# Kernel optimization log

Hardware: AMD Instinct MI355X
Metric: run time of the kernel (lower is better)

The kernel has to match this reference:

```python
import jax, jax.numpy as jnp
import numpy as np

B, C, S, DIM = 8, 3, 1024, 768
H = 3
HD = DIM // H  # 256


def setup_inputs() -> dict:
    key = jax.random.key(0)
    ks = jax.random.split(key, 7)
    s = 1.0 / np.sqrt(HD)  # torch Linear default init scale
    return {
        "linear_embed": jax.random.normal(ks[0], (B, C, S, DIM), dtype=jnp.float32),
        "Wq": jax.random.uniform(ks[1], (H, HD, HD), jnp.float32, -s, s),
        "bq": jax.random.uniform(ks[2], (H, HD), jnp.float32, -s, s),
        "Wk": jax.random.uniform(ks[3], (H, HD, HD), jnp.float32, -s, s),
        "bk": jax.random.uniform(ks[4], (H, HD), jnp.float32, -s, s),
        "Wv": jax.random.uniform(ks[5], (H, HD, HD), jnp.float32, -s, s),
        "bv": jax.random.uniform(ks[6], (H, HD), jnp.float32, -s, s),
    }


def reference(linear_embed, Wq, bq, Wk, bk, Wv, bv):
    # Split last dim into heads: [B, C, S, H, HD]
    x = linear_embed.reshape(B, C, S, H, HD)
    # Per-head Linear: y = x @ W.T + b (torch convention, W is [out, in])
    q = jnp.einsum("bcshd,hed->bcshe", x, Wq) + bq
    k = jnp.einsum("bcshd,hed->bcshe", x, Wk) + bk
    v = jnp.einsum("bcshd,hed->bcshe", x, Wv) + bv
    scale = 1.0 / np.sqrt(HD)
    scores = jnp.einsum("bcshe,bcthe->bchst", q, k) * scale  # [B,C,H,S,S]
    attn = jax.nn.softmax(scores, axis=-1)
    out = jnp.einsum("bchst,bcthe->bcshe", attn, v)  # [B,C,S,H,HD]
    # hstack over heads -> [B,C,S,DIM]; hstack over channels -> [B,S,C*DIM]
    out = out.reshape(B, C, S, DIM)
    return jnp.transpose(out, (0, 2, 1, 3)).reshape(B, S, C * DIM)
```

## Files before the change

### kernel.cpp

```cpp
#include <hip/hip_runtime.h>

#define Bn 8
#define Cn 3
#define Sn 1024
#define DIMn 768
#define Hn 3
#define HDn 256
#define BCHn 72
#define SnHD (Sn*HDn)

typedef __bf16 bf16x8 __attribute__((ext_vector_type(8)));
typedef float f32x4 __attribute__((ext_vector_type(4)));
typedef unsigned short u16x8 __attribute__((ext_vector_type(8)));
typedef unsigned short u16x4 __attribute__((ext_vector_type(4)));

static __device__ __forceinline__ unsigned short f2bf(float f){
  unsigned u = __builtin_bit_cast(unsigned, f);
  u += 0x7fffu + ((u >> 16) & 1u);
  return (unsigned short)(u >> 16);
}
static __device__ __forceinline__ u16x4 cvt4(float4 v){
  u16x4 r = { f2bf(v.x), f2bf(v.y), f2bf(v.z), f2bf(v.w) };
  return r;
}
static __device__ __forceinline__ bf16x8 ld8(const unsigned short* p){
  return __builtin_bit_cast(bf16x8, *(const u16x8*)p);
}
static __device__ __forceinline__ float fexp2(float x){
#if __has_builtin(__builtin_amdgcn_exp2f)
  return __builtin_amdgcn_exp2f(x);
#else
  return exp2f(x);
#endif
}

#if __has_builtin(__builtin_amdgcn_global_load_lds)
#define HAVE_ASYNC 1
static __device__ __forceinline__ void async16(const void* g, void* l){
  __builtin_amdgcn_global_load_lds((const __attribute__((address_space(1))) void*)g,
                                   (__attribute__((address_space(3))) void*)l, 16, 0, 0);
}
#else
#define HAVE_ASYNC 0
#endif

__global__ __launch_bounds__(256) void wprep(
    const float* __restrict__ Wq, const float* __restrict__ Wk, const float* __restrict__ Wv,
    unsigned short* __restrict__ Wb)
{
  const int which = blockIdx.z, h = blockIdx.y;
  const float* src = which == 0 ? Wq : (which == 1 ? Wk : Wv);
  const float scale = (which == 0) ? 0.09016844136545405f : 1.0f;
  const int off = blockIdx.x*1024 + threadIdx.x*4;
  float4 v = *(const float4*)(src + (long)h*65536 + off);
  v.x *= scale; v.y *= scale; v.z *= scale; v.w *= scale;
  *(u16x4*)(Wb + (long)(which*Hn + h)*65536 + off) = cvt4(v);
}

__global__ __launch_bounds__(256, 2) void projkv(
    const float* __restrict__ x, const unsigned short* __restrict__ Wb,
    const float* __restrict__ bk, const float* __restrict__ bv,
    unsigned short* __restrict__ Kw, unsigned short* __restrict__ Vt)
{
  __shared__ alignas(16) unsigned short SM[23040];
  unsigned short* XA  = SM;
  unsigned short* WkL = SM + 2560;
  unsigned short* WvL = SM + 12800;
  unsigned short* TK  = SM;
  unsigned short* TV  = SM;

  const int tid = threadIdx.x, lane = tid & 63, wave = tid >> 6;
  const int l15 = lane & 15, quad = lane >> 4;
  const int bch = blockIdx.y;
  const int h = bch % Hn, c = (bch / Hn) % Cn, b = bch / (Hn*Cn);
  const int tb = blockIdx.x * 64;
  const long xb_ = ((long)(b*Cn + c)*Sn + tb)*DIMn + h*HDn;
  const unsigned short* Wkb = Wb + (long)(1*Hn + h)*65536;
  const unsigned short* Wvb = Wb + (long)(2*Hn + h)*65536;

  float4 xr[2]; u16x8 wk[4], wv[4];
  auto loadg = [&](int ks){
    const int k0 = ks*32;
    #pragma unroll
    for (int i = 0; i < 2; ++i){
      int id = tid + i*256;
      xr[i] = *(const float4*)(x + xb_ + (long)(id>>3)*DIMn + k0 + (id&7)*4);
    }
    #pragma unroll
    for (int i = 0; i < 4; ++i){
      int id = tid + i*256;
      wk[i] = *(const u16x8*)(Wkb + (id>>2)*HDn + k0 + (id&3)*8);
      wv[i] = *(const u16x8*)(Wvb + (id>>2)*HDn + k0 + (id&3)*8);
    }
  };
  loadg(0);

  f32x4 Ka[16] = {}; f32x4 Va[4][4] = {};
  for (int ks = 0; ks < 8; ++ks){
    #pragma unroll
    for (int i = 0; i < 2; ++i){
      int id = tid + i*256;
      *(u16x4*)&XA[(id>>3)*40 + (id&7)*4] = cvt4(xr[i]);
    }
    #pragma unroll
    for (int i = 0; i < 4; ++i){
      int id = tid + i*256;
      *(u16x8*)&WkL[(id>>2)*40 + (id&3)*8] = wk[i];
      *(u16x8*)&WvL[(id>>2)*40 + (id&3)*8] = wv[i];
    }
    __syncthreads();
    if (ks < 7) loadg(ks + 1);
    bf16x8 af = ld8(&XA[(wave*16 + l15)*40 + quad*8]);
    #pragma unroll
    for (int nt = 0; nt < 16; ++nt){
      bf16x8 bw = ld8(&WkL[(nt*16 + l15)*40 + quad*8]);
      Ka[nt] = __builtin_amdgcn_mfma_f32_16x16x32_bf16(af, bw, Ka[nt], 0, 0, 0);
    }
    bf16x8 avf[4], bxf[4];
    #pragma unroll
    for (int j = 0; j < 4; ++j) avf[j] = ld8(&WvL[((wave*4 + j)*16 + l15)*40 + quad*8]);
    #pragma unroll
    for (int n = 0; n < 4; ++n) bxf[n] = ld8(&XA[(n*16 + l15)*40 + quad*8]);
    #pragma unroll
    for (int j = 0; j < 4; ++j)
      #pragma unroll
      for (int n = 0; n < 4; ++n)
        Va[j][n] = __builtin_amdgcn_mfma_f32_16x16x32_bf16(avf[j], bxf[n], Va[j][n], 0, 0, 0);
    __syncthreads();
  }

  const float* bkh = bk + h*HDn;
  const float* bvh = bv + h*HDn;
  #pragma unroll
  for (int nt = 0; nt < 16; ++nt){
    const float bb = bkh[nt*16 + l15];
    #pragma unroll
    for (int r = 0; r < 4; ++r)
      TK[(wave*16 + quad*4 + r)*264 + nt*16 + l15] = f2bf(Ka[nt][r] + bb);
  }
  __syncthreads();
  unsigned short* Kg = Kw + (long)bch*SnHD + (long)tb*HDn;
  #pragma unroll
  for (int i = 0; i < 8; ++i){
    int id = tid + i*256, row = id>>5, c8 = (id&31)*8;
    *(u16x8*)(Kg + row*HDn + c8) = *(const u16x8*)&TK[row*264 + c8];
  }
  __syncthreads();
  #pragma unroll
  for (int j = 0; j < 4; ++j){
    #pragma unroll
    for (int n = 0; n < 4; ++n){
      #pragma unroll
      for (int r = 0; r < 4; ++r){
        const int er = wave*64 + j*16 + quad*4 + r;
        TV[er*72 + n*16 + l15] = f2bf(Va[j][n][r] + bvh[er]);
      }
    }
  }
  __syncthreads();
  unsigned short* Vg = Vt + (long)bch*SnHD + tb;
  #pragma unroll
  for (int i = 0; i < 8; ++i){
    int id = tid + i*256, row = id>>3, c8 = (id&7)*8;
    *(u16x8*)(Vg + (long)row*Sn + c8) = *(const u16x8*)&TV[row*72 + c8];
  }
}

__global__ __launch_bounds__(256, 3) void attn(
    const float* __restrict__ x, const unsigned short* __restrict__ Wb,
    const float* __restrict__ bq,
    const unsigned short* __restrict__ Kw, const unsigned short* __restrict__ Vt,
    float* __restrict__ out)
{
  __shared__ alignas(16) unsigned short SM[21632];
  unsigned short* XA = SM;
  unsigned short* WL = SM + 2560;
  unsigned short* KL = SM;
  unsigned short* VL = SM + 8192;
  unsigned short* PL = SM + 19072;

  const int tid = threadIdx.x, lane = tid & 63, wave = tid >> 6;
  const int l15 = lane & 15, quad = lane >> 4;
  const int bid = blockIdx.x;
  const int idx0 = bid >> 3;
  const int bch = (idx0 >> 4)*8 + (bid & 7);
  const int qt  = idx0 & 15;
  const int h = bch % Hn, c = (bch / Hn) % Cn, b = bch / (Hn*Cn);
  const int q0 = qt * 64;
  const long xb_ = ((long)(b*Cn + c)*Sn + q0)*DIMn + h*HDn;
  const unsigned short* Wqb = Wb + (long)h*65536;

  float4 xr[2]; u16x8 wr[4];
  auto loadgA = [&](int ks){
    const int k0 = ks*32;
    #pragma unroll
    for (int i = 0; i < 2; ++i){
      int id = tid + i*256;
      xr[i] = *(const float4*)(x + xb_ + (long)(id>>3)*DIMn + k0 + (id&7)*4);
    }
    #pragma unroll
    for (int i = 0; i < 4; ++i){
      int id = tid + i*256;
      wr[i] = *(const u16x8*)(Wqb + (id>>2)*HDn + k0 + (id&3)*8);
    }
  };
  loadgA(0);
  f32x4 qa[16] = {};
  for (int ks = 0; ks < 8; ++ks){
    #pragma unroll
    for (int i = 0; i < 2; ++i){
      int id = tid + i*256;
      *(u16x4*)&XA[(id>>3)*40 + (id&7)*4] = cvt4(xr[i]);
    }
    #pragma unroll
    for (int i = 0; i < 4; ++i){
      int id = tid + i*256;
      *(u16x8*)&WL[(id>>2)*40 + (id&3)*8] = wr[i];
    }
    __syncthreads();
    if (ks < 7) loadgA(ks + 1);
    bf16x8 af = ld8(&XA[(wave*16 + l15)*40 + quad*8]);
    #pragma unroll
    for (int nt = 0; nt < 16; ++nt){
      bf16x8 bw = ld8(&WL[(nt*16 + l15)*40 + quad*8]);
      qa[nt] = __builtin_amdgcn_mfma_f32_16x16x32_bf16(af, bw, qa[nt], 0, 0, 0);
    }
    __syncthreads();
  }

  const unsigned short* Kb = Kw + (long)bch*SnHD;
  const unsigned short* Vb = Vt + (long)bch*SnHD;

#if HAVE_ASYNC
  auto issueK = [&](int jt){
    const int t0 = jt*32;
    #pragma unroll
    for (int i = 0; i < 4; ++i){
      const int S = (wave*4 + i)*64 + lane;
      const int row = S >> 5, pos = S & 31, ch = pos ^ (row & 15);
      async16(Kb + (long)(t0 + row)*HDn + ch*8, (char*)KL + (wave*4 + i)*1024);
    }
  };
  issueK(0);
#else
  u16x8 kr_[4];
  auto loadK = [&](int jt){
    const int t0 = jt*32;
    #pragma unroll
    for (int i = 0; i < 4; ++i){
      const int S = (wave*4 + i)*64 + lane;
      const int row = S >> 5, pos = S & 31, ch = pos ^ (row & 15);
      kr_[i] = *(const u16x8*)(Kb + (long)(t0 + row)*HDn + ch*8);
    }
  };
  loadK(0);
#endif

  unsigned short* Pw = PL + wave*640;
  const float s2 = 0.09016844136545405f;
  bf16x8 qf[8];
  #pragma unroll
  for (int g = 0; g < 8; ++g){
    #pragma unroll
    for (int e2 = 0; e2 < 2; ++e2){
      const int nt = g*2 + e2;
      const float bias = bq[h*HDn + nt*16 + l15] * s2;
      #pragma unroll
      for (int r = 0; r < 4; ++r)
        Pw[(quad*4 + r)*40 + e2*16 + l15] = f2bf(qa[nt][r] + bias);
    }
    qf[g] = ld8(&Pw[l15*40 + quad*8]);
  }

  if (tid < 128){
    const int row = 256 + (tid >> 3), c4 = (tid & 7)*4;
    const unsigned short vv = (row == 256) ? (unsigned short)0x3F80 : (unsigned short)0;
    u16x4 z = { vv, vv, vv, vv };
    *(u16x4*)&VL[row*40 + c4] = z;
  }

  u16x8 vr[4];
  auto loadV = [&](int jt){
    const int t0 = jt*32;
    #pragma unroll
    for (int i = 0; i < 4; ++i){
      int id = tid + i*256;
      vr[i] = *(const u16x8*)(Vb + (long)(id>>2)*Sn + t0 + (id&3)*8);
    }
  };
  loadV(0);

  f32x4 o[17] = {};
  for (int jt = 0; jt < 32; ++jt){
    #pragma unroll
    for (int i = 0; i < 4; ++i){
      int id = tid + i*256;
      *(u16x8*)&VL[(id>>2)*40 + (id&3)*8] = vr[i];
    }
#if !HAVE_ASYNC
    #pragma unroll
    for (int i = 0; i < 4; ++i){
      const int S = (wave*4 + i)*64 + lane;
      *(u16x8*)&KL[S*8] = kr_[i];
    }
#endif
    __syncthreads();
    if (jt < 31){
      loadV(jt + 1);
#if !HAVE_ASYNC
      loadK(jt + 1);
#endif
    }
    f32x4 s0 = {}, s1 = {};
    #pragma unroll
    for (int kk = 0; kk < 8; ++kk){
      const int pc = 4*kk + quad;
      bf16x8 b0 = ld8(&KL[l15*256 + (pc ^ l15)*8]);
      bf16x8 b1 = ld8(&KL[(16 + l15)*256 + (pc ^ l15)*8]);
      s0 = __builtin_amdgcn_mfma_f32_16x16x32_bf16(qf[kk], b0, s0, 0, 0, 0);
      s1 = __builtin_amdgcn_mfma_f32_16x16x32_bf16(qf[kk], b1, s1, 0, 0, 0);
    }
    #pragma unroll
    for (int r = 0; r < 4; ++r){
      Pw[(quad*4 + r)*40 + l15]      = f2bf(fexp2(s0[r]));
      Pw[(quad*4 + r)*40 + 16 + l15] = f2bf(fexp2(s1[r]));
    }
    bf16x8 pf = ld8(&Pw[l15*40 + quad*8]);
    #pragma unroll
    for (int nt = 0; nt < 17; ++nt){
      bf16x8 vf = ld8(&VL[(nt*16 + l15)*40 + quad*8]);
      o[nt] = __builtin_amdgcn_mfma_f32_16x16x32_bf16(pf, vf, o[nt], 0, 0, 0);
    }
    __syncthreads();
#if HAVE_ASYNC
    if (jt < 31) issueK(jt + 1);
#endif
  }

  #pragma unroll
  for (int r = 0; r < 4; ++r){
    const float l = __shfl(o[16][r], lane & 48);
    const float inv = 1.0f / l;
    const int grow = q0 + wave*16 + quad*4 + r;
    float* op = out + ((long)(b*Sn + grow)*Cn + c)*DIMn + h*HDn;
    #pragma unroll
    for (int nt = 0; nt < 16; ++nt)
      op[nt*16 + l15] = o[nt][r] * inv;
  }
}

extern "C" void kernel_launch(void* const* d_in, const int* in_sizes, int n_in,
                              void* d_out, int out_size, void* d_ws, size_t ws_size,
                              hipStream_t stream) {
  const float* x  = (const float*)d_in[0];
  const float* Wq = (const float*)d_in[1];
  const float* bq = (const float*)d_in[2];
  const float* Wk = (const float*)d_in[3];
  const float* bk = (const float*)d_in[4];
  const float* Wv = (const float*)d_in[5];
  const float* bv = (const float*)d_in[6];
  float* out = (float*)d_out;
  unsigned short* Kw = (unsigned short*)d_ws;
  unsigned short* Vt = Kw + (size_t)BCHn * SnHD;
  unsigned short* Wb = Vt + (size_t)BCHn * SnHD;

  wprep<<<dim3(64, Hn, 3), 256, 0, stream>>>(Wq, Wk, Wv, Wb);
  projkv<<<dim3(16, BCHn), 256, 0, stream>>>(x, Wb, bk, bv, Kw, Vt);
  attn<<<dim3(BCHn * 16), 256, 0, stream>>>(x, Wb, bq, Kw, Vt, out);
}
```

Before: 333.1 us.

## Rework attention kernel to 32x32 MFMA tiles with pre-swizzled K/V layouts

Switches the attention kernel from 16x16x32 to 32x32x16 MFMA tiles, raising the query tile to 128 rows per block (32 per wave). projkv and wprep now write K, V and Wq in a fragment-ready swizzled global layout, so they can be streamed straight into double-buffered LDS with async loads. The softmax row sum is now accumulated in registers, replacing the extra ones-column MFMA. Output goes through an LDS transpose for coalesced float4 stores. Occupancy drops to 2 blocks per CU with larger LDS use, and the grid is halved, which may hurt latency hiding.

```diff
diff --git a/kernel.cpp b/kernel.cpp
--- a/kernel.cpp
+++ b/kernel.cpp
@@ -11,19 +11,25 @@
 
 typedef __bf16 bf16x8 __attribute__((ext_vector_type(8)));
 typedef float f32x4 __attribute__((ext_vector_type(4)));
+typedef float f32x16 __attribute__((ext_vector_type(16)));
 typedef unsigned short u16x8 __attribute__((ext_vector_type(8)));
 typedef unsigned short u16x4 __attribute__((ext_vector_type(4)));
+typedef unsigned u32x2 __attribute__((ext_vector_type(2)));
+typedef unsigned u32x4 __attribute__((ext_vector_type(4)));
 
 static __device__ __forceinline__ unsigned short f2bf(float f){
   unsigned u = __builtin_bit_cast(unsigned, f);
   u += 0x7fffu + ((u >> 16) & 1u);
   return (unsigned short)(u >> 16);
 }
+static __device__ __forceinline__ unsigned pk2(float a, float b){
+  return (unsigned)f2bf(a) | ((unsigned)f2bf(b) << 16);
+}
 static __device__ __forceinline__ u16x4 cvt4(float4 v){
   u16x4 r = { f2bf(v.x), f2bf(v.y), f2bf(v.z), f2bf(v.w) };
   return r;
 }
-static __device__ __forceinline__ bf16x8 ld8(const unsigned short* p){
+static __device__ __forceinline__ bf16x8 ld8(const void* p){
   return __builtin_bit_cast(bf16x8, *(const u16x8*)p);
 }
 static __device__ __forceinline__ float fexp2(float x){
@@ -43,6 +49,22 @@
 #else
 #define HAVE_ASYNC 0
 #endif
+
+static __device__ __forceinline__ bf16x8 pack8(const float* t, int hi){
+  unsigned A0 = pk2(t[0], t[1]), A1 = pk2(t[2], t[3]);
+  unsigned B0 = pk2(t[4], t[5]), B1 = pk2(t[6], t[7]);
+#if __has_builtin(__builtin_amdgcn_permlane32_swap)
+  u32x2 r0 = __builtin_amdgcn_permlane32_swap(A0, B0, false, false);
+  u32x2 r1 = __builtin_amdgcn_permlane32_swap(A1, B1, false, false);
+  u32x4 w = { r0[0], r1[0], r0[1], r1[1] };
+#else
+  unsigned sA0 = (unsigned)__shfl_xor((int)A0, 32), sA1 = (unsigned)__shfl_xor((int)A1, 32);
+  unsigned sB0 = (unsigned)__shfl_xor((int)B0, 32), sB1 = (unsigned)__shfl_xor((int)B1, 32);
+  u32x4 w = { hi ? sB0 : A0, hi ? sB1 : A1, hi ? B0 : sA0, hi ? B1 : sA1 };
+#endif
+  (void)hi;
+  return __builtin_bit_cast(bf16x8, w);
+}
 
 __global__ __launch_bounds__(256) void wprep(
     const float* __restrict__ Wq, const float* __restrict__ Wk, const float* __restrict__ Wv,
@@ -54,7 +76,15 @@
   const int off = blockIdx.x*1024 + threadIdx.x*4;
   float4 v = *(const float4*)(src + (long)h*65536 + off);
   v.x *= scale; v.y *= scale; v.z *= scale; v.w *= scale;
-  *(u16x4*)(Wb + (long)(which*Hn + h)*65536 + off) = cvt4(v);
+  long o;
+  if (which == 0){
+    const int e = off >> 8, k0 = off & 255;
+    const int ks = k0 >> 6, kst = (k0 >> 4) & 3, hb = (k0 >> 3) & 1, j0 = k0 & 7;
+    o = (long)h*65536 + ks*16384 + ((e>>5)*4 + kst)*512 + (((hb<<5)|(e&31))*8) + j0;
+  } else {
+    o = (long)(which*Hn + h)*65536 + off;
+  }
+  *(u16x4*)(Wb + o) = cvt4(v);
 }
 
 __global__ __launch_bounds__(256, 2) void projkv(
@@ -139,11 +169,15 @@
       TK[(wave*16 + quad*4 + r)*264 + nt*16 + l15] = f2bf(Ka[nt][r] + bb);
   }
   __syncthreads();
-  unsigned short* Kg = Kw + (long)bch*SnHD + (long)tb*HDn;
-  #pragma unroll
-  for (int i = 0; i < 8; ++i){
-    int id = tid + i*256, row = id>>5, c8 = (id&31)*8;
-    *(u16x8*)(Kg + row*HDn + c8) = *(const u16x8*)&TK[row*264 + c8];
+  {
+    unsigned short* Kg = Kw + (long)bch*SnHD + (long)(tb>>5)*8192;
+    #pragma unroll
+    for (int i = 0; i < 8; ++i){
+      const int f = wave*8 + i;
+      const int tl = f >> 4, kc = f & 15;
+      *(u16x8*)(Kg + (long)tl*8192 + kc*512 + lane*8) =
+        *(const u16x8*)&TK[(tl*32 + (lane&31))*264 + kc*16 + (lane>>5)*8];
+    }
   }
   __syncthreads();
   #pragma unroll
@@ -158,194 +192,188 @@
     }
   }
   __syncthreads();
-  unsigned short* Vg = Vt + (long)bch*SnHD + tb;
-  #pragma unroll
-  for (int i = 0; i < 8; ++i){
-    int id = tid + i*256, row = id>>3, c8 = (id&7)*8;
-    *(u16x8*)(Vg + (long)row*Sn + c8) = *(const u16x8*)&TV[row*72 + c8];
-  }
-}
-
-__global__ __launch_bounds__(256, 3) void attn(
+  {
+    unsigned short* Vg = Vt + (long)bch*SnHD + (long)(tb>>5)*8192;
+    #pragma unroll
+    for (int i = 0; i < 8; ++i){
+      const int f = wave*8 + i;
+      const int tcl = f >> 4, r2 = f & 15;
+      *(u16x8*)(Vg + (long)tcl*8192 + r2*512 + lane*8) =
+        *(const u16x8*)&TV[((r2>>1)*32 + (lane&31))*72 + tcl*32 + (r2&1)*16 + (lane>>5)*8];
+    }
+  }
+}
+
+__global__ __launch_bounds__(256, 2) void attn(
     const float* __restrict__ x, const unsigned short* __restrict__ Wb,
     const float* __restrict__ bq,
     const unsigned short* __restrict__ Kw, const unsigned short* __restrict__ Vt,
     float* __restrict__ out)
 {
-  __shared__ alignas(16) unsigned short SM[21632];
-  unsigned short* XA = SM;
-  unsigned short* WL = SM + 2560;
-  unsigned short* KL = SM;
-  unsigned short* VL = SM + 8192;
-  unsigned short* PL = SM + 19072;
+  __shared__ alignas(16) char SM[66560];
 
   const int tid = threadIdx.x, lane = tid & 63, wave = tid >> 6;
-  const int l15 = lane & 15, quad = lane >> 4;
+  const int l31 = lane & 31, hi = lane >> 5;
   const int bid = blockIdx.x;
-  const int idx0 = bid >> 3;
-  const int bch = (idx0 >> 4)*8 + (bid & 7);
-  const int qt  = idx0 & 15;
+  const int g = bid >> 3;
+  const int bch = (g & ~7) | (bid & 7);
+  const int qt = g & 7;
   const int h = bch % Hn, c = (bch / Hn) % Cn, b = bch / (Hn*Cn);
-  const int q0 = qt * 64;
+  const int q0 = qt * 128;
   const long xb_ = ((long)(b*Cn + c)*Sn + q0)*DIMn + h*HDn;
-  const unsigned short* Wqb = Wb + (long)h*65536;
-
-  float4 xr[2]; u16x8 wr[4];
-  auto loadgA = [&](int ks){
-    const int k0 = ks*32;
-    #pragma unroll
-    for (int i = 0; i < 2; ++i){
-      int id = tid + i*256;
-      xr[i] = *(const float4*)(x + xb_ + (long)(id>>3)*DIMn + k0 + (id&7)*4);
-    }
-    #pragma unroll
-    for (int i = 0; i < 4; ++i){
-      int id = tid + i*256;
-      wr[i] = *(const u16x8*)(Wqb + (id>>2)*HDn + k0 + (id&3)*8);
+
+  float* bql = (float*)(SM + 65536);
+  bql[tid] = bq[h*HDn + tid] * 0.09016844136545405f;
+
+  float4 xv[4][2];
+  auto loadX = [&](int ks){
+    #pragma unroll
+    for (int i = 0; i < 4; ++i){
+      const int vid = tid + i*256;
+      const int q = vid >> 3, kg = vid & 7;
+      const float* p = x + xb_ + (long)q*DIMn + ks*64 + kg*8;
+      xv[i][0] = *(const float4*)p;
+      xv[i][1] = *(const float4*)(p + 4);
     }
   };
-  loadgA(0);
-  f32x4 qa[16] = {};
-  for (int ks = 0; ks < 8; ++ks){
-    #pragma unroll
-    for (int i = 0; i < 2; ++i){
-      int id = tid + i*256;
-      *(u16x4*)&XA[(id>>3)*40 + (id&7)*4] = cvt4(xr[i]);
-    }
-    #pragma unroll
-    for (int i = 0; i < 4; ++i){
-      int id = tid + i*256;
-      *(u16x8*)&WL[(id>>2)*40 + (id&3)*8] = wr[i];
-    }
-    __syncthreads();
-    if (ks < 7) loadgA(ks + 1);
-    bf16x8 af = ld8(&XA[(wave*16 + l15)*40 + quad*8]);
-    #pragma unroll
-    for (int nt = 0; nt < 16; ++nt){
-      bf16x8 bw = ld8(&WL[(nt*16 + l15)*40 + quad*8]);
-      qa[nt] = __builtin_amdgcn_mfma_f32_16x16x32_bf16(af, bw, qa[nt], 0, 0, 0);
+  const unsigned short* Wq2 = Wb + (long)h*65536;
+  auto issueW = [&](int ks){
+    #pragma unroll
+    for (int i = 0; i < 8; ++i){
+      const int f = wave*8 + i;
+#if HAVE_ASYNC
+      async16(Wq2 + (long)ks*16384 + f*512 + lane*8, SM + 16384 + f*1024);
+#else
+      *(u16x8*)(SM + 16384 + f*1024 + lane*16) =
+          *(const u16x8*)(Wq2 + (long)ks*16384 + f*512 + lane*8);
+#endif
+    }
+  };
+  loadX(0);
+  f32x16 acc[8] = {};
+  for (int ks = 0; ks < 4; ++ks){
+    #pragma unroll
+    for (int i = 0; i < 4; ++i){
+      const int vid = tid + i*256;
+      const int q = vid >> 3, kg = vid & 7;
+      u16x4 lo = cvt4(xv[i][0]), hh = cvt4(xv[i][1]);
+      u16x8 w = { lo[0], lo[1], lo[2], lo[3], hh[0], hh[1], hh[2], hh[3] };
+      *(u16x8*)(SM + q*128 + ((kg*16) ^ ((q & 7) << 4))) = w;
+    }
+    issueW(ks);
+    __syncthreads();
+    if (ks < 3) loadX(ks + 1);
+    #pragma unroll
+    for (int kst = 0; kst < 4; ++kst){
+      bf16x8 xb = ld8(SM + (wave*32 + l31)*128 + ((kst*32 + hi*16) ^ ((l31 & 7) << 4)));
+      #pragma unroll
+      for (int et = 0; et < 8; ++et){
+        bf16x8 af = ld8(SM + 16384 + (et*4 + kst)*1024 + lane*16);
+        acc[et] = __builtin_amdgcn_mfma_f32_32x32x16_bf16(af, xb, acc[et], 0, 0, 0);
+      }
     }
     __syncthreads();
   }
 
   const unsigned short* Kb = Kw + (long)bch*SnHD;
   const unsigned short* Vb = Vt + (long)bch*SnHD;
-
+  auto stageKV = [&](int jt, int buf){
+    const long kb2 = (long)jt * 8192;
+    #pragma unroll
+    for (int i = 0; i < 4; ++i){
+      const int f = wave*4 + i;
 #if HAVE_ASYNC
-  auto issueK = [&](int jt){
-    const int t0 = jt*32;
-    #pragma unroll
-    for (int i = 0; i < 4; ++i){
-      const int S = (wave*4 + i)*64 + lane;
-      const int row = S >> 5, pos = S & 31, ch = pos ^ (row & 15);
-      async16(Kb + (long)(t0 + row)*HDn + ch*8, (char*)KL + (wave*4 + i)*1024);
+      async16(Kb + kb2 + f*512 + lane*8, SM + buf*16384 + f*1024);
+#else
+      *(u16x8*)(SM + buf*16384 + f*1024 + lane*16) = *(const u16x8*)(Kb + kb2 + f*512 + lane*8);
+#endif
+    }
+    #pragma unroll
+    for (int i = 0; i < 4; ++i){
+      const int f = wave*4 + i;
+#if HAVE_ASYNC
+      async16(Vb + kb2 + f*512 + lane*8, SM + 32768 + buf*16384 + f*1024);
+#else
+      *(u16x8*)(SM + 32768 + buf*16384 + f*1024 + lane*16) = *(const u16x8*)(Vb + kb2 + f*512 + lane*8);
+#endif
     }
   };
-  issueK(0);
-#else
-  u16x8 kr_[4];
-  auto loadK = [&](int jt){
-    const int t0 = jt*32;
-    #pragma unroll
-    for (int i = 0; i < 4; ++i){
-      const int S = (wave*4 + i)*64 + lane;
-      const int row = S >> 5, pos = S & 31, ch = pos ^ (row & 15);
-      kr_[i] = *(const u16x8*)(Kb + (long)(t0 + row)*HDn + ch*8);
-    }
-  };
-  loadK(0);
-#endif
-
-  unsigned short* Pw = PL + wave*640;
-  const float s2 = 0.09016844136545405f;
-  bf16x8 qf[8];
-  #pragma unroll
-  for (int g = 0; g < 8; ++g){
-    #pragma unroll
-    for (int e2 = 0; e2 < 2; ++e2){
-      const int nt = g*2 + e2;
-      const float bias = bq[h*HDn + nt*16 + l15] * s2;
+  stageKV(0, 0);
+
+  bf16x8 qf[16];
+  #pragma unroll
+  for (int et = 0; et < 8; ++et){
+    float t[16];
+    #pragma unroll
+    for (int G = 0; G < 4; ++G){
+      f32x4 bb = *(const f32x4*)&bql[et*32 + 8*G + 4*hi];
+      t[4*G+0] = acc[et][4*G+0] + bb[0];
+      t[4*G+1] = acc[et][4*G+1] + bb[1];
+      t[4*G+2] = acc[et][4*G+2] + bb[2];
+      t[4*G+3] = acc[et][4*G+3] + bb[3];
+    }
+    qf[2*et]   = pack8(t,     hi);
+    qf[2*et+1] = pack8(t + 8, hi);
+  }
+  __syncthreads();
+
+  f32x16 o[8] = {};
+  float lsum = 0.f;
+  #pragma unroll 2
+  for (int jt = 0; jt < 32; ++jt){
+    const int buf = jt & 1;
+    if (jt < 31) stageKV(jt + 1, buf ^ 1);
+    f32x16 s = {};
+    const char* KLb = SM + buf*16384 + lane*16;
+    #pragma unroll
+    for (int kc = 0; kc < 16; ++kc){
+      bf16x8 kf = ld8(KLb + kc*1024);
+      s = __builtin_amdgcn_mfma_f32_32x32x16_bf16(kf, qf[kc], s, 0, 0, 0);
+    }
+    float p[16];
+    #pragma unroll
+    for (int i = 0; i < 16; ++i) p[i] = fexp2(s[i]);
+    lsum += (((p[0]+p[1])+(p[2]+p[3])) + ((p[4]+p[5])+(p[6]+p[7])))
+          + (((p[8]+p[9])+(p[10]+p[11])) + ((p[12]+p[13])+(p[14]+p[15])));
+    bf16x8 pB0 = pack8(p, hi), pB1 = pack8(p + 8, hi);
+    const char* VLb = SM + 32768 + buf*16384 + lane*16;
+    #pragma unroll
+    for (int et = 0; et < 8; ++et){
+      bf16x8 v0 = ld8(VLb + (et*2+0)*1024);
+      o[et] = __builtin_amdgcn_mfma_f32_32x32x16_bf16(v0, pB0, o[et], 0, 0, 0);
+      bf16x8 v1 = ld8(VLb + (et*2+1)*1024);
+      o[et] = __builtin_amdgcn_mfma_f32_32x32x16_bf16(v1, pB1, o[et], 0, 0, 0);
+    }
+    __syncthreads();
+  }
+
+  const float lt = lsum + __shfl_xor(lsum, 32);
+  const float inv = 1.0f / lt;
+  #pragma unroll
+  for (int et = 0; et < 8; ++et)
+    #pragma unroll
+    for (int r = 0; r < 16; ++r) o[et][r] *= inv;
+
+  char* TB = SM + wave*16384;
+  #pragma unroll
+  for (int pass = 0; pass < 2; ++pass){
+    #pragma unroll
+    for (int e2 = 0; e2 < 4; ++e2){
+      const int et = pass*4 + e2;
       #pragma unroll
-      for (int r = 0; r < 4; ++r)
-        Pw[(quad*4 + r)*40 + e2*16 + l15] = f2bf(qa[nt][r] + bias);
-    }
-    qf[g] = ld8(&Pw[l15*40 + quad*8]);
-  }
-
-  if (tid < 128){
-    const int row = 256 + (tid >> 3), c4 = (tid & 7)*4;
-    const unsigned short vv = (row == 256) ? (unsigned short)0x3F80 : (unsigned short)0;
-    u16x4 z = { vv, vv, vv, vv };
-    *(u16x4*)&VL[row*40 + c4] = z;
-  }
-
-  u16x8 vr[4];
-  auto loadV = [&](int jt){
-    const int t0 = jt*32;
-    #pragma unroll
-    for (int i = 0; i < 4; ++i){
-      int id = tid + i*256;
-      vr[i] = *(const u16x8*)(Vb + (long)(id>>2)*Sn + t0 + (id&3)*8);
-    }
-  };
-  loadV(0);
-
-  f32x4 o[17] = {};
-  for (int jt = 0; jt < 32; ++jt){
-    #pragma unroll
-    for (int i = 0; i < 4; ++i){
-      int id = tid + i*256;
-      *(u16x8*)&VL[(id>>2)*40 + (id&3)*8] = vr[i];
-    }
-#if !HAVE_ASYNC
-    #pragma unroll
-    for (int i = 0; i < 4; ++i){
-      const int S = (wave*4 + i)*64 + lane;
-      *(u16x8*)&KL[S*8] = kr_[i];
-    }
-#endif
-    __syncthreads();
-    if (jt < 31){
-      loadV(jt + 1);
-#if !HAVE_ASYNC
-      loadK(jt + 1);
-#endif
-    }
-    f32x4 s0 = {}, s1 = {};
-    #pragma unroll
-    for (int kk = 0; kk < 8; ++kk){
-      const int pc = 4*kk + quad;
-      bf16x8 b0 = ld8(&KL[l15*256 + (pc ^ l15)*8]);
-      bf16x8 b1 = ld8(&KL[(16 + l15)*256 + (pc ^ l15)*8]);
-      s0 = __builtin_amdgcn_mfma_f32_16x16x32_bf16(qf[kk], b0, s0, 0, 0, 0);
-      s1 = __builtin_amdgcn_mfma_f32_16x16x32_bf16(qf[kk], b1, s1, 0, 0, 0);
-    }
-    #pragma unroll
-    for (int r = 0; r < 4; ++r){
-      Pw[(quad*4 + r)*40 + l15]      = f2bf(fexp2(s0[r]));
-      Pw[(quad*4 + r)*40 + 16 + l15] = f2bf(fexp2(s1[r]));
-    }
-    bf16x8 pf = ld8(&Pw[l15*40 + quad*8]);
-    #pragma unroll
-    for (int nt = 0; nt < 17; ++nt){
-      bf16x8 vf = ld8(&VL[(nt*16 + l15)*40 + quad*8]);
-      o[nt] = __builtin_amdgcn_mfma_f32_16x16x32_bf16(pf, vf, o[nt], 0, 0, 0);
-    }
-    __syncthreads();
-#if HAVE_ASYNC
-    if (jt < 31) issueK(jt + 1);
-#endif
-  }
-
-  #pragma unroll
-  for (int r = 0; r < 4; ++r){
-    const float l = __shfl(o[16][r], lane & 48);
-    const float inv = 1.0f / l;
-    const int grow = q0 + wave*16 + quad*4 + r;
-    float* op = out + ((long)(b*Sn + grow)*Cn + c)*DIMn + h*HDn;
-    #pragma unroll
-    for (int nt = 0; nt < 16; ++nt)
-      op[nt*16 + l15] = o[nt][r] * inv;
+      for (int G = 0; G < 4; ++G){
+        f32x4 w = { o[et][4*G+0], o[et][4*G+1], o[et][4*G+2], o[et][4*G+3] };
+        const int el0 = e2*32 + 8*G + 4*hi;
+        *(f32x4*)(TB + l31*512 + ((el0*4) ^ ((l31 & 7) << 4))) = w;
+      }
+    }
+    #pragma unroll
+    for (int i = 0; i < 16; ++i){
+      const int qr = i*2 + hi;
+      f32x4 v = *(const f32x4*)(TB + qr*512 + ((l31*16) ^ ((qr & 7) << 4)));
+      float* op = out + ((long)(b*Sn + q0 + wave*32 + qr)*Cn + c)*DIMn + h*HDn + pass*128 + l31*4;
+      *(f32x4*)op = v;
+    }
   }
 }
 
@@ -366,5 +394,5 @@
 
   wprep<<<dim3(64, Hn, 3), 256, 0, stream>>>(Wq, Wk, Wv, Wb);
   projkv<<<dim3(16, BCHn), 256, 0, stream>>>(x, Wb, bk, bv, Kw, Vt);
-  attn<<<dim3(BCHn * 16), 256, 0, stream>>>(x, Wb, bq, Kw, Vt, out);
-}
+  attn<<<dim3(BCHn * 8), 256, 0, stream>>>(x, Wb, bq, Kw, Vt, out);
+}
```

Measured after the change: 304.3 us. 1.09x faster.
